# Performance work log

Hardware: AMD Instinct MI355X
Metric: run time of the kernel (lower is better)

The kernel has to match this reference:

```python
import jax, jax.numpy as jnp
import numpy as np

N_HEADS = 16
ROPE_BASE = 10000.0


def _rope_tables(T, head_dim, dtype):
    d2 = head_dim // 2
    inv_freq = 1.0 / (ROPE_BASE ** (jnp.arange(0, head_dim, 2, dtype=jnp.float32) / head_dim))
    t = jnp.arange(T, dtype=jnp.float32)
    freqs = jnp.outer(t, inv_freq)  # [T, d2]
    cos = jnp.cos(freqs)[None, :, None, :].astype(dtype)  # [1,T,1,d2]
    sin = jnp.sin(freqs)[None, :, None, :].astype(dtype)
    return cos, sin


def _apply_rotary(x, cos, sin):
    # x: [B,T,H,D]; rotate halves
    d = x.shape[-1] // 2
    x1, x2 = x[..., :d], x[..., d:]
    return jnp.concatenate([x1 * cos + x2 * sin, -x1 * sin + x2 * cos], axis=-1)


def setup_inputs() -> dict:
    key = jax.random.key(0)
    k1, k2, k3 = jax.random.split(key, 3)
    B, T, C = 2, 2048, 1024
    x = jax.random.normal(k1, (B, T, C), dtype=jnp.float32)
    w_attn = jax.random.normal(k2, (3 * C, C), dtype=jnp.float32) * (1.0 / np.sqrt(C))
    w_proj = jax.random.normal(k3, (C, C), dtype=jnp.float32) * (1.0 / np.sqrt(C))
    return {"x": x, "w_attn": w_attn, "w_proj": w_proj}


def reference(x, w_attn, w_proj):
    B, T, C = x.shape
    H = N_HEADS
    D = C // H
    qkv = jnp.einsum('btc,fc->btf', x, w_attn)  # [B,T,3C]
    q, k, v = jnp.split(qkv, 3, axis=2)
    q = q.reshape(B, T, H, D)
    k = k.reshape(B, T, H, D)
    v = v.reshape(B, T, H, D)
    cos, sin = _rope_tables(T, D, x.dtype)
    q = _apply_rotary(q, cos, sin)
    k = _apply_rotary(k, cos, sin)
    # causal SDPA, scale 1/sqrt(D)
    scale = 1.0 / np.sqrt(D)
    scores = jnp.einsum('bqhd,bkhd->bhqk', q, k) * scale
    causal = jnp.tril(jnp.ones((T, T), dtype=bool))
    scores = jnp.where(causal[None, None], scores, jnp.finfo(scores.dtype).min)
    attn = jax.nn.softmax(scores, axis=-1)
    y = jnp.einsum('bhqk,bkhd->bqhd', attn, v).reshape(B, T, C)
    return jnp.einsum('btc,oc->bto', y, w_proj)
```

## Files before the change

kernel.cpp:

```cpp
#include <hip/hip_runtime.h>
#include <math.h>

typedef __bf16 bf16x8 __attribute__((ext_vector_type(8)));
typedef float f32x4 __attribute__((ext_vector_type(4)));

__device__ __forceinline__ unsigned f2bf(float f) {
    union { float f; unsigned u; } v; v.f = f;
    return (v.u + 0x7FFFu + ((v.u >> 16) & 1u)) >> 16;
}

__device__ __forceinline__ unsigned cvtpk(float a, float b) {
    unsigned r;
    __asm__("v_cvt_pk_bf16_f32 %0, %1, %2" : "=v"(r) : "v"(a), "v"(b));
    return r;
}

__device__ __forceinline__ void gload16(const ushort* g, ushort* l) {
    __builtin_amdgcn_global_load_lds(
        (const __attribute__((address_space(1))) void*)g,
        (__attribute__((address_space(3))) void*)l, 16, 0, 0);
}

__device__ __forceinline__ bool src_is_fp32(const unsigned* s) {
    int sane = 0;
#pragma unroll
    for (int i = 0; i < 64; ++i) {
        unsigned lo = s[i] & 0xFFFFu;
        unsigned e = (lo >> 7) & 0xFF;
        if (lo == 0u || (e >= 100u && e <= 140u)) sane++;
    }
    return sane < 48;
}

__global__ __launch_bounds__(256) void tobf16_all_kernel(
    const unsigned* __restrict__ s0, const unsigned* __restrict__ s1,
    const unsigned* __restrict__ s2,
    ushort* __restrict__ d0, ushort* __restrict__ d1, ushort* __restrict__ d2) {
    const int bx = blockIdx.x;
    const unsigned* src;
    ushort* dst;
    int lb;
    if (bx < 2048)      { src = s0; dst = d0; lb = bx; }
    else if (bx < 3584) { src = s1; dst = d1; lb = bx - 2048; }
    else                { src = s2; dst = d2; lb = bx - 3584; }
    const int i = lb * 2048 + threadIdx.x * 8;
    if (src_is_fp32(src)) {
        const float* fs = (const float*)src;
        float4 f0 = *(const float4*)(fs + i);
        float4 f1 = *(const float4*)(fs + i + 4);
        uint4 o;
        o.x = f2bf(f0.x) | (f2bf(f0.y) << 16);
        o.y = f2bf(f0.z) | (f2bf(f0.w) << 16);
        o.z = f2bf(f1.x) | (f2bf(f1.y) << 16);
        o.w = f2bf(f1.z) | (f2bf(f1.w) << 16);
        *(uint4*)(dst + i) = o;
    } else {
        *(uint4*)(dst + i) = *(const uint4*)((const ushort*)src + i);
    }
}

constexpr int GBM = 128, GBN = 128, GBK = 32;

__global__ __launch_bounds__(256) void gemm_qkv_rope_kernel(
    const ushort* __restrict__ A, const ushort* __restrict__ Bmat,
    ushort* __restrict__ qkvh, int K) {
    __shared__ ushort As[2][GBM * GBK];
    __shared__ ushort Bs[2][GBN * GBK];

    const int tid  = threadIdx.x;
    const int lane = tid & 63;
    const int wv   = tid >> 6;
    const int wm   = (wv >> 1) * 64;
    const int wn   = (wv & 1) * 64;

    const ushort* Ab = A + (size_t)blockIdx.x * GBM * K;
    const ushort* Bb = Bmat + (size_t)blockIdx.y * GBN * K;

    f32x4 acc[4][4];
#pragma unroll
    for (int i = 0; i < 4; i++)
#pragma unroll
        for (int j = 0; j < 4; j++) acc[i][j] = (f32x4){0.f, 0.f, 0.f, 0.f};

    const int srow = tid >> 2;
    const int scol = (tid & 3) * 8;
    const int fr = lane & 15;
    const int fk = (lane >> 4) * 8;
    const int nK = K >> 5;

    gload16(Ab + (size_t)srow * K + scol,        As[0] + wv * 512);
    gload16(Ab + (size_t)(srow + 64) * K + scol, As[0] + wv * 512 + 2048);
    gload16(Bb + (size_t)srow * K + scol,        Bs[0] + wv * 512);
    gload16(Bb + (size_t)(srow + 64) * K + scol, Bs[0] + wv * 512 + 2048);

#pragma unroll 1
    for (int it = 0; it < nK; ++it) {
        const int cur = it & 1;
        __syncthreads();
        if (it + 1 < nK) {
            const int k0 = (it + 1) << 5, nxt = cur ^ 1;
            gload16(Ab + (size_t)srow * K + k0 + scol,        As[nxt] + wv * 512);
            gload16(Ab + (size_t)(srow + 64) * K + k0 + scol, As[nxt] + wv * 512 + 2048);
            gload16(Bb + (size_t)srow * K + k0 + scol,        Bs[nxt] + wv * 512);
            gload16(Bb + (size_t)(srow + 64) * K + k0 + scol, Bs[nxt] + wv * 512 + 2048);
        }
        bf16x8 af[4], bfr[4];
#pragma unroll
        for (int i = 0; i < 4; i++)
            af[i] = *(const bf16x8*)(As[cur] + (wm + i * 16 + fr) * GBK + fk);
#pragma unroll
        for (int j = 0; j < 4; j++)
            bfr[j] = *(const bf16x8*)(Bs[cur] + (wn + j * 16 + fr) * GBK + fk);
#pragma unroll
        for (int i = 0; i < 4; i++)
#pragma unroll
            for (int j = 0; j < 4; j++)
                acc[i][j] = __builtin_amdgcn_mfma_f32_16x16x32_bf16(af[i], bfr[j], acc[i][j], 0, 0, 0);
    }

    const int crow0 = (lane >> 4) * 4;
    const int col0  = blockIdx.y * GBN + wn;
    const int which = col0 >> 10;
    const int hh    = (col0 >> 6) & 15;

    if (which < 2) {
        ushort* outp = qkvh + (size_t)which * 4194304 + (size_t)hh * 131072;
        const float inva = exp2f((float)fr * -0.41524101186f);
        const float invb = exp2f((float)(fr + 16) * -0.41524101186f);
        const float qs = (which == 0) ? 0.125f : 1.0f;
#pragma unroll
        for (int i = 0; i < 4; i++)
#pragma unroll
            for (int r = 0; r < 4; r++) {
                int row = blockIdx.x * GBM + wm + i * 16 + crow0 + r;
                int t = row & 2047;
                size_t ob = ((size_t)(row >> 11)) * 2097152 + (size_t)t * 64;
                float sa, ca, sb, cb;
                __sincosf((float)t * inva, &sa, &ca);
                __sincosf((float)t * invb, &sb, &cb);
                float q0 = acc[i][0][r], q1 = acc[i][1][r];
                float q2 = acc[i][2][r], q3 = acc[i][3][r];
                float n0 = (q0 * ca + q2 * sa) * qs;
                float n1 = (q1 * cb + q3 * sb) * qs;
                float n2 = (q2 * ca - q0 * sa) * qs;
                float n3 = (q3 * cb - q1 * sb) * qs;
                unsigned u01 = cvtpk(n0, n1);
                unsigned u23 = cvtpk(n2, n3);
                outp[ob + fr]      = (ushort)(u01 & 0xFFFFu);
                outp[ob + 16 + fr] = (ushort)(u01 >> 16);
                outp[ob + 32 + fr] = (ushort)(u23 & 0xFFFFu);
                outp[ob + 48 + fr] = (ushort)(u23 >> 16);
            }
    } else {
        const int row0 = blockIdx.x * GBM;
        ushort* vout = qkvh + (size_t)2 * 4194304
                     + ((size_t)(row0 >> 11)) * 2097152 + (size_t)hh * 131072;
#pragma unroll
        for (int i = 0; i < 4; i++) {
            const int t0 = (blockIdx.x * GBM + wm + i * 16 + crow0) & 2047;
#pragma unroll
            for (int j = 0; j < 4; j++) {
                uint2 u;
                u.x = cvtpk(acc[i][j][0], acc[i][j][1]);
                u.y = cvtpk(acc[i][j][2], acc[i][j][3]);
                *(uint2*)(vout + (size_t)(j * 16 + fr) * 2048 + t0) = u;
            }
        }
    }
}

__global__ __launch_bounds__(256) void gemm_bt_kernel(
    const ushort* __restrict__ A, const ushort* __restrict__ Bmat,
    float* __restrict__ C, int M, int N, int K) {
    __shared__ ushort As[2][GBM * GBK];
    __shared__ ushort Bs[2][GBN * GBK];

    const int tid  = threadIdx.x;
    const int lane = tid & 63;
    const int wv   = tid >> 6;
    const int wm   = (wv >> 1) * 64;
    const int wn   = (wv & 1) * 64;

    const ushort* Ab = A + (size_t)blockIdx.x * GBM * K;
    const ushort* Bb = Bmat + (size_t)blockIdx.y * GBN * K;

    f32x4 acc[4][4];
#pragma unroll
    for (int i = 0; i < 4; i++)
#pragma unroll
        for (int j = 0; j < 4; j++) acc[i][j] = (f32x4){0.f, 0.f, 0.f, 0.f};

    const int srow = tid >> 2;
    const int scol = (tid & 3) * 8;
    const int fr = lane & 15;
    const int fk = (lane >> 4) * 8;
    const int nK = K >> 5;

    gload16(Ab + (size_t)srow * K + scol,        As[0] + wv * 512);
    gload16(Ab + (size_t)(srow + 64) * K + scol, As[0] + wv * 512 + 2048);
    gload16(Bb + (size_t)srow * K + scol,        Bs[0] + wv * 512);
    gload16(Bb + (size_t)(srow + 64) * K + scol, Bs[0] + wv * 512 + 2048);

#pragma unroll 1
    for (int it = 0; it < nK; ++it) {
        const int cur = it & 1;
        __syncthreads();
        if (it + 1 < nK) {
            const int k0 = (it + 1) << 5, nxt = cur ^ 1;
            gload16(Ab + (size_t)srow * K + k0 + scol,        As[nxt] + wv * 512);
            gload16(Ab + (size_t)(srow + 64) * K + k0 + scol, As[nxt] + wv * 512 + 2048);
            gload16(Bb + (size_t)srow * K + k0 + scol,        Bs[nxt] + wv * 512);
            gload16(Bb + (size_t)(srow + 64) * K + k0 + scol, Bs[nxt] + wv * 512 + 2048);
        }
        bf16x8 af[4], bfr[4];
#pragma unroll
        for (int i = 0; i < 4; i++)
            af[i] = *(const bf16x8*)(As[cur] + (wm + i * 16 + fr) * GBK + fk);
#pragma unroll
        for (int j = 0; j < 4; j++)
            bfr[j] = *(const bf16x8*)(Bs[cur] + (wn + j * 16 + fr) * GBK + fk);
#pragma unroll
        for (int i = 0; i < 4; i++)
#pragma unroll
            for (int j = 0; j < 4; j++)
                acc[i][j] = __builtin_amdgcn_mfma_f32_16x16x32_bf16(af[i], bfr[j], acc[i][j], 0, 0, 0);
    }

    const int crow0 = (lane >> 4) * 4;
#pragma unroll
    for (int i = 0; i < 4; i++)
#pragma unroll
        for (int j = 0; j < 4; j++)
#pragma unroll
            for (int r = 0; r < 4; r++) {
                int row = blockIdx.x * GBM + wm + i * 16 + crow0 + r;
                int col = blockIdx.y * GBN + wn + j * 16 + fr;
                C[(size_t)row * N + col] = acc[i][j][r];
            }
}

#define NEG_BIG (-1e30f)
constexpr int LPP    = 72;
constexpr int VT_OFF = 16384;
constexpr int PS_OFF = 32768;

__global__ __launch_bounds__(512) void attn_kernel(const ushort* __restrict__ qkvh,
                                                   ushort* __restrict__ y) {
    __shared__ ushort SM[PS_OFF + 8 * 32 * LPP];

    const int tid  = threadIdx.x;
    const int lane = tid & 63;
    const int wv   = tid >> 6;
    const int half = wv >> 2;
    const int wq   = wv & 3;
    const int jb   = half * 4;
    const int pid  = blockIdx.x;
    const int bh   = blockIdx.y;
    const int b    = bh >> 4, h = bh & 15;

    const ushort* qp = qkvh + (size_t)b * 2097152 + (size_t)h * 131072;
    const ushort* kp = qp + 4194304;
    const ushort* vp = qp + 8388608;

    const int fr = lane & 15;
    const int fq = lane >> 4;
    const int fk = fq * 8;

    const int ksrcA = (tid >> 3) * 64 + (((tid & 7) ^ ((tid >> 3) & 7)) << 3);
    const int ksrcB = ksrcA + 4096;
    const int vsrcA = (tid >> 4) * 2048 + (((tid & 15) ^ ((tid >> 4) & 15)) << 3);
    const int vsrcB = vsrcA + 65536;
    const int koff0 = (fq ^ (fr & 7)) << 3;
    const int koff1 = koff0 ^ 32;
    const int voff0 = ((half * 8 + fq) ^ fr) << 3;
    const int voff1 = ((half * 8 + 4 + fq) ^ fr) << 3;

    ushort* pw = SM + PS_OFF + wv * (32 * LPP);

#pragma unroll 1
    for (int seg = 0; seg < 2; ++seg) {
        const int qb = seg ? (15 - pid) : pid;
        const int nIt = qb + 1;

        __syncthreads();

        gload16(kp + ksrcA, SM + wv * 512);
        gload16(kp + ksrcB, SM + 4096 + wv * 512);
        gload16(vp + vsrcA, SM + VT_OFF + wv * 512);
        gload16(vp + vsrcB, SM + VT_OFF + 4096 + wv * 512);

        const int qrowA = qb * 128 + wq * 32 + fr;
        bf16x8 qfA0 = *(const bf16x8*)(qp + (size_t)qrowA * 64 + fk);
        bf16x8 qfA1 = *(const bf16x8*)(qp + (size_t)qrowA * 64 + 32 + fk);
        bf16x8 qfB0 = *(const bf16x8*)(qp + (size_t)(qrowA + 16) * 64 + fk);
        bf16x8 qfB1 = *(const bf16x8*)(qp + (size_t)(qrowA + 16) * 64 + 32 + fk);

        f32x4 oA[4], oB[4];
#pragma unroll
        for (int j4 = 0; j4 < 4; ++j4) {
            oA[j4] = (f32x4){0.f, 0.f, 0.f, 0.f};
            oB[j4] = (f32x4){0.f, 0.f, 0.f, 0.f};
        }
        float lsumA = 0.f, lsumB = 0.f;

#pragma unroll 1
        for (int it = 0; it < nIt; ++it) {
            const int cur = it & 1;
            const int k0 = it * 128;
            const ushort* Ksc = SM + cur * 8192;
            const ushort* Vtc = SM + VT_OFF + cur * 8192;
            __syncthreads();
            if (it + 1 < nIt) {
                const int nxt = cur ^ 1;
                gload16(kp + (it + 1) * 8192 + ksrcA, SM + nxt * 8192 + wv * 512);
                gload16(kp + (it + 1) * 8192 + ksrcB, SM + nxt * 8192 + 4096 + wv * 512);
                gload16(vp + (it + 1) * 128 + vsrcA, SM + VT_OFF + nxt * 8192 + wv * 512);
                gload16(vp + (it + 1) * 128 + vsrcB, SM + VT_OFF + nxt * 8192 + 4096 + wv * 512);
            }

            f32x4 sA[4], sB[4];
#pragma unroll
            for (int jl = 0; jl < 4; ++jl) {
                const int row = ((jb + jl) * 16 + fr) * 64;
                bf16x8 kf0 = *(const bf16x8*)(Ksc + row + koff0);
                bf16x8 kf1 = *(const bf16x8*)(Ksc + row + koff1);
                f32x4 zA = (f32x4){0.f, 0.f, 0.f, 0.f};
                f32x4 zB = (f32x4){0.f, 0.f, 0.f, 0.f};
                zA = __builtin_amdgcn_mfma_f32_16x16x32_bf16(kf0, qfA0, zA, 0, 0, 0);
                zA = __builtin_amdgcn_mfma_f32_16x16x32_bf16(kf1, qfA1, zA, 0, 0, 0);
                zB = __builtin_amdgcn_mfma_f32_16x16x32_bf16(kf0, qfB0, zB, 0, 0, 0);
                zB = __builtin_amdgcn_mfma_f32_16x16x32_bf16(kf1, qfB1, zB, 0, 0, 0);
                sA[jl] = zA;
                sB[jl] = zB;
            }
            if (it + 1 < nIt) {
#pragma unroll
                for (int jl = 0; jl < 4; ++jl)
#pragma unroll
                    for (int r = 0; r < 4; ++r) {
                        float pA = __expf(sA[jl][r]);
                        float pB = __expf(sB[jl][r]);
                        sA[jl][r] = pA; lsumA += pA;
                        sB[jl][r] = pB; lsumB += pB;
                    }
            } else {
#pragma unroll
                for (int jl = 0; jl < 4; ++jl)
#pragma unroll
                    for (int r = 0; r < 4; ++r) {
                        const int key = k0 + (jb + jl) * 16 + fq * 4 + r;
                        float vA = (key > qrowA)      ? NEG_BIG : sA[jl][r];
                        float vB = (key > qrowA + 16) ? NEG_BIG : sB[jl][r];
                        float pA = __expf(vA);
                        float pB = __expf(vB);
                        sA[jl][r] = pA; lsumA += pA;
                        sB[jl][r] = pB; lsumB += pB;
                    }
            }

#pragma unroll
            for (int jl = 0; jl < 4; ++jl) {
                uint2 uA, uB;
                uA.x = cvtpk(sA[jl][0], sA[jl][1]);
                uA.y = cvtpk(sA[jl][2], sA[jl][3]);
                uB.x = cvtpk(sB[jl][0], sB[jl][1]);
                uB.y = cvtpk(sB[jl][2], sB[jl][3]);
                *(uint2*)(pw + fr * LPP + jl * 16 + fq * 4)        = uA;
                *(uint2*)(pw + (16 + fr) * LPP + jl * 16 + fq * 4) = uB;
            }
            __asm__ volatile("" ::: "memory");

#pragma unroll
            for (int kl = 0; kl < 2; ++kl) {
                bf16x8 pfA = *(const bf16x8*)(pw + fr * LPP + kl * 32 + fk);
                bf16x8 pfB = *(const bf16x8*)(pw + (16 + fr) * LPP + kl * 32 + fk);
                const int voff = kl ? voff1 : voff0;
#pragma unroll
                for (int j4 = 0; j4 < 4; ++j4) {
                    bf16x8 vf = *(const bf16x8*)(Vtc + (j4 * 16 + fr) * 128 + voff);
                    oA[j4] = __builtin_amdgcn_mfma_f32_16x16x32_bf16(pfA, vf, oA[j4], 0, 0, 0);
                    oB[j4] = __builtin_amdgcn_mfma_f32_16x16x32_bf16(pfB, vf, oB[j4], 0, 0, 0);
                }
            }
        }

        lsumA += __shfl_xor(lsumA, 16, 64);
        lsumA += __shfl_xor(lsumA, 32, 64);
        lsumB += __shfl_xor(lsumB, 16, 64);
        lsumB += __shfl_xor(lsumB, 32, 64);

        __syncthreads();
        float* exA = (float*)(SM + PS_OFF) + (wq * 2) * 1104;
        float* exB = exA + 1104;
        if (half) {
#pragma unroll
            for (int j4 = 0; j4 < 4; ++j4)
#pragma unroll
                for (int r = 0; r < 4; ++r) {
                    exA[lane * 17 + j4 * 4 + r] = oA[j4][r];
                    exB[lane * 17 + j4 * 4 + r] = oB[j4][r];
                }
            if (fq == 0) {
                exA[1088 + fr] = lsumA;
                exB[1088 + fr] = lsumB;
            }
        }
        __syncthreads();
        if (!half) {
            float linvA[4], linvB[4];
#pragma unroll
            for (int r = 0; r < 4; ++r) {
                float ownA = __shfl(lsumA, fq * 4 + r, 64);
                float ownB = __shfl(lsumB, fq * 4 + r, 64);
                linvA[r] = 1.0f / (ownA + exA[1088 + fq * 4 + r]);
                linvB[r] = 1.0f / (ownB + exB[1088 + fq * 4 + r]);
            }
#pragma unroll
            for (int j4 = 0; j4 < 4; j4 += 2)
#pragma unroll
                for (int r = 0; r < 4; ++r) {
                    int rowA = qb * 128 + wq * 32 + fq * 4 + r;
                    size_t ybA = ((size_t)b * 2048 + rowA) * 1024 + h * 64;
                    float a0 = (oA[j4][r]     + exA[lane * 17 + j4 * 4 + r])       * linvA[r];
                    float a1 = (oA[j4 + 1][r] + exA[lane * 17 + (j4 + 1) * 4 + r]) * linvA[r];
                    unsigned ua = cvtpk(a0, a1);
                    y[ybA + j4 * 16 + fr]       = (ushort)(ua & 0xFFFFu);
                    y[ybA + (j4 + 1) * 16 + fr] = (ushort)(ua >> 16);

                    size_t ybB = ybA + (size_t)16 * 1024;
                    float b0 = (oB[j4][r]     + exB[lane * 17 + j4 * 4 + r])       * linvB[r];
                    float b1 = (oB[j4 + 1][r] + exB[lane * 17 + (j4 + 1) * 4 + r]) * linvB[r];
                    unsigned ub = cvtpk(b0, b1);
                    y[ybB + j4 * 16 + fr]       = (ushort)(ub & 0xFFFFu);
                    y[ybB + (j4 + 1) * 16 + fr] = (ushort)(ub >> 16);
                }
        }
    }
}

extern "C" void kernel_launch(void* const* d_in, const int* in_sizes, int n_in,
                              void* d_out, int out_size, void* d_ws, size_t ws_size,
                              hipStream_t stream) {
    const int nx = in_sizes[0];
    const int na = in_sizes[1];
    const int np = in_sizes[2];

    ushort* qkvh = (ushort*)d_ws;
    ushort* yb   = qkvh + (size_t)3 * 4194304;
    ushort* xb   = yb + (size_t)4096 * 1024;
    ushort* wab  = xb + nx;
    ushort* wpb  = wab + na;
    size_t need = ((size_t)3 * 4194304 + (size_t)4096 * 1024 + nx + na + np) * 2;
    if (ws_size < need) return;

    tobf16_all_kernel<<<dim3(4096), 256, 0, stream>>>(
        (const unsigned*)d_in[0], (const unsigned*)d_in[1], (const unsigned*)d_in[2],
        xb, wab, wpb);

    gemm_qkv_rope_kernel<<<dim3(32, 24), 256, 0, stream>>>(xb, wab, qkvh, 1024);
    attn_kernel<<<dim3(8, 32), 512, 0, stream>>>(qkvh, yb);
    gemm_bt_kernel<<<dim3(32, 8), 256, 0, stream>>>(yb, wpb, (float*)d_out, 4096, 1024, 1024);
}
```

Before: 180.5 us.

## Halve attention query tile to 64 rows with 256-thread blocks

```diff
diff --git a/kernel.cpp b/kernel.cpp
--- a/kernel.cpp
+++ b/kernel.cpp
@@ -244,15 +244,15 @@
 constexpr int VT_OFF = 16384;
 constexpr int PS_OFF = 32768;
 
-__global__ __launch_bounds__(512) void attn_kernel(const ushort* __restrict__ qkvh,
+__global__ __launch_bounds__(256) void attn_kernel(const ushort* __restrict__ qkvh,
                                                    ushort* __restrict__ y) {
-    __shared__ ushort SM[PS_OFF + 8 * 32 * LPP];
+    __shared__ ushort SM[PS_OFF + 4 * 16 * LPP];
 
     const int tid  = threadIdx.x;
     const int lane = tid & 63;
     const int wv   = tid >> 6;
-    const int half = wv >> 2;
-    const int wq   = wv & 3;
+    const int half = wv >> 1;
+    const int wq   = wv & 1;
     const int jb   = half * 4;
     const int pid  = blockIdx.x;
     const int bh   = blockIdx.y;
@@ -267,29 +267,28 @@
     const int fk = fq * 8;
 
     const int ksrcA = (tid >> 3) * 64 + (((tid & 7) ^ ((tid >> 3) & 7)) << 3);
-    const int ksrcB = ksrcA + 4096;
     const int vsrcA = (tid >> 4) * 2048 + (((tid & 15) ^ ((tid >> 4) & 15)) << 3);
-    const int vsrcB = vsrcA + 65536;
     const int koff0 = (fq ^ (fr & 7)) << 3;
     const int koff1 = koff0 ^ 32;
     const int voff0 = ((half * 8 + fq) ^ fr) << 3;
     const int voff1 = ((half * 8 + 4 + fq) ^ fr) << 3;
 
-    ushort* pw = SM + PS_OFF + wv * (32 * LPP);
+    ushort* pw = SM + PS_OFF + wv * (16 * LPP);
 
 #pragma unroll 1
     for (int seg = 0; seg < 2; ++seg) {
-        const int qb = seg ? (15 - pid) : pid;
-        const int nIt = qb + 1;
+        const int qb = seg ? (31 - pid) : pid;
+        const int nIt = (qb >> 1) + 1;
 
         __syncthreads();
 
-        gload16(kp + ksrcA, SM + wv * 512);
-        gload16(kp + ksrcB, SM + 4096 + wv * 512);
-        gload16(vp + vsrcA, SM + VT_OFF + wv * 512);
-        gload16(vp + vsrcB, SM + VT_OFF + 4096 + wv * 512);
-
-        const int qrowA = qb * 128 + wq * 32 + fr;
+#pragma unroll
+        for (int i = 0; i < 4; ++i) {
+            gload16(kp + i * 2048 + ksrcA, SM + i * 2048 + wv * 512);
+            gload16(vp + i * 32768 + vsrcA, SM + VT_OFF + i * 2048 + wv * 512);
+        }
+
+        const int qrowA = qb * 64 + wq * 32 + fr;
         bf16x8 qfA0 = *(const bf16x8*)(qp + (size_t)qrowA * 64 + fk);
         bf16x8 qfA1 = *(const bf16x8*)(qp + (size_t)qrowA * 64 + 32 + fk);
         bf16x8 qfB0 = *(const bf16x8*)(qp + (size_t)(qrowA + 16) * 64 + fk);
@@ -312,11 +311,17 @@
             __syncthreads();
             if (it + 1 < nIt) {
                 const int nxt = cur ^ 1;
-                gload16(kp + (it + 1) * 8192 + ksrcA, SM + nxt * 8192 + wv * 512);
-                gload16(kp + (it + 1) * 8192 + ksrcB, SM + nxt * 8192 + 4096 + wv * 512);
-                gload16(vp + (it + 1) * 128 + vsrcA, SM + VT_OFF + nxt * 8192 + wv * 512);
-                gload16(vp + (it + 1) * 128 + vsrcB, SM + VT_OFF + nxt * 8192 + 4096 + wv * 512);
-            }
+#pragma unroll
+                for (int i = 0; i < 4; ++i) {
+                    gload16(kp + (it + 1) * 8192 + i * 2048 + ksrcA,
+                            SM + nxt * 8192 + i * 2048 + wv * 512);
+                    gload16(vp + (it + 1) * 128 + i * 32768 + vsrcA,
+                            SM + VT_OFF + nxt * 8192 + i * 2048 + wv * 512);
+                }
+            }
+
+            const bool lastIt = (it + 1 == nIt);
+            if (lastIt && ((qb & 1) == 0) && half) continue;
 
             f32x4 sA[4], sB[4];
 #pragma unroll
@@ -333,7 +338,7 @@
                 sA[jl] = zA;
                 sB[jl] = zB;
             }
-            if (it + 1 < nIt) {
+            if (!lastIt) {
 #pragma unroll
                 for (int jl = 0; jl < 4; ++jl)
 #pragma unroll
@@ -358,29 +363,46 @@
                     }
             }
 
+            bf16x8 vf[2][4];
+#pragma unroll
+            for (int kl = 0; kl < 2; ++kl) {
+                const int voff = kl ? voff1 : voff0;
+#pragma unroll
+                for (int j4 = 0; j4 < 4; ++j4)
+                    vf[kl][j4] = *(const bf16x8*)(Vtc + (j4 * 16 + fr) * 128 + voff);
+            }
+
 #pragma unroll
             for (int jl = 0; jl < 4; ++jl) {
-                uint2 uA, uB;
+                uint2 uA;
                 uA.x = cvtpk(sA[jl][0], sA[jl][1]);
                 uA.y = cvtpk(sA[jl][2], sA[jl][3]);
+                *(uint2*)(pw + fr * LPP + jl * 16 + fq * 4) = uA;
+            }
+            __asm__ volatile("" ::: "memory");
+#pragma unroll
+            for (int kl = 0; kl < 2; ++kl) {
+                bf16x8 pfA = *(const bf16x8*)(pw + fr * LPP + kl * 32 + fk);
+#pragma unroll
+                for (int j4 = 0; j4 < 4; ++j4)
+                    oA[j4] = __builtin_amdgcn_mfma_f32_16x16x32_bf16(pfA, vf[kl][j4], oA[j4], 0, 0, 0);
+            }
+            __asm__ volatile("" ::: "memory");
+
+#pragma unroll
+            for (int jl = 0; jl < 4; ++jl) {
+                uint2 uB;
                 uB.x = cvtpk(sB[jl][0], sB[jl][1]);
                 uB.y = cvtpk(sB[jl][2], sB[jl][3]);
-                *(uint2*)(pw + fr * LPP + jl * 16 + fq * 4)        = uA;
-                *(uint2*)(pw + (16 + fr) * LPP + jl * 16 + fq * 4) = uB;
+                *(uint2*)(pw + fr * LPP + jl * 16 + fq * 4) = uB;
             }
             __asm__ volatile("" ::: "memory");
-
 #pragma unroll
             for (int kl = 0; kl < 2; ++kl) {
-                bf16x8 pfA = *(const bf16x8*)(pw + fr * LPP + kl * 32 + fk);
-                bf16x8 pfB = *(const bf16x8*)(pw + (16 + fr) * LPP + kl * 32 + fk);
-                const int voff = kl ? voff1 : voff0;
-#pragma unroll
-                for (int j4 = 0; j4 < 4; ++j4) {
-                    bf16x8 vf = *(const bf16x8*)(Vtc + (j4 * 16 + fr) * 128 + voff);
-                    oA[j4] = __builtin_amdgcn_mfma_f32_16x16x32_bf16(pfA, vf, oA[j4], 0, 0, 0);
-                    oB[j4] = __builtin_amdgcn_mfma_f32_16x16x32_bf16(pfB, vf, oB[j4], 0, 0, 0);
-                }
+                bf16x8 pfB = *(const bf16x8*)(pw + fr * LPP + kl * 32 + fk);
+#pragma unroll
+                for (int j4 = 0; j4 < 4; ++j4)
+                    oB[j4] = __builtin_amdgcn_mfma_f32_16x16x32_bf16(pfB, vf[kl][j4], oB[j4], 0, 0, 0);
             }
         }
 
@@ -390,7 +412,7 @@
         lsumB += __shfl_xor(lsumB, 32, 64);
 
         __syncthreads();
-        float* exA = (float*)(SM + PS_OFF) + (wq * 2) * 1104;
+        float* exA = (float*)SM + (wq * 2) * 1104;
         float* exB = exA + 1104;
         if (half) {
 #pragma unroll
@@ -419,7 +441,7 @@
             for (int j4 = 0; j4 < 4; j4 += 2)
 #pragma unroll
                 for (int r = 0; r < 4; ++r) {
-                    int rowA = qb * 128 + wq * 32 + fq * 4 + r;
+                    int rowA = qb * 64 + wq * 32 + fq * 4 + r;
                     size_t ybA = ((size_t)b * 2048 + rowA) * 1024 + h * 64;
                     float a0 = (oA[j4][r]     + exA[lane * 17 + j4 * 4 + r])       * linvA[r];
                     float a1 = (oA[j4 + 1][r] + exA[lane * 17 + (j4 + 1) * 4 + r]) * linvA[r];
@@ -458,6 +480,6 @@
         xb, wab, wpb);
 
     gemm_qkv_rope_kernel<<<dim3(32, 24), 256, 0, stream>>>(xb, wab, qkvh, 1024);
-    attn_kernel<<<dim3(8, 32), 512, 0, stream>>>(qkvh, yb);
+    attn_kernel<<<dim3(16, 32), 256, 0, stream>>>(qkvh, yb);
     gemm_bt_kernel<<<dim3(32, 8), 256, 0, stream>>>(yb, wpb, (float*)d_out, 4096, 1024, 1024);
 }
```

Result: slower. 194.1 us (+7.6%).
